# Performance work log

Measured on AMD Instinct MI355X. Metric: run time of the kernel, lower is better.

The kernel has to match this reference:

```python
import jax, jax.numpy as jnp
import numpy as np

B, S, C, H = 256, 512, 64, 128  # batch, seq_len, input channels, LSTM hidden


def setup_inputs() -> dict:
    key = jax.random.key(0)
    ks = jax.random.split(key, 9)
    s = 1.0 / np.sqrt(H)  # torch nn.LSTM init: U(-1/sqrt(H), 1/sqrt(H))
    u = lambda k, shape: jax.random.uniform(k, shape, jnp.float32, -s, s)
    return {
        "x": jax.random.normal(ks[0], (B, S, C), jnp.float32),
        # layer 0 (input size C)
        "Wih0": u(ks[1], (4 * H, C)),
        "Whh0": u(ks[2], (4 * H, H)),
        "bih0": u(ks[3], (4 * H,)),
        "bhh0": u(ks[4], (4 * H,)),
        # layer 1 (input size H)
        "Wih1": u(ks[5], (4 * H, H)),
        "Whh1": u(ks[6], (4 * H, H)),
        "bih1": u(ks[7], (4 * H,)),
        "bhh1": u(ks[8], (4 * H,)),
    }


def _lstm_layer(x, Wih, Whh, bih, bhh):
    """x: (S, B, in) -> outputs h_t for all t: (S, B, H). Torch gate order i,f,g,o."""
    Hh = Whh.shape[1]
    # Input-to-hidden GEMM hoisted out of the recurrence (batched over S).
    xg = jnp.einsum('sbc,gc->sbg', x, Wih) + bih + bhh  # (S, B, 4H)

    def step(carry, xt):
        h, c = carry
        g = xt + h @ Whh.T  # (B, 4H)
        i, f, gg, o = jnp.split(g, 4, axis=-1)
        i = jax.nn.sigmoid(i)
        f = jax.nn.sigmoid(f)
        gg = jnp.tanh(gg)
        o = jax.nn.sigmoid(o)
        c = f * c + i * gg
        h = o * jnp.tanh(c)
        return (h, c), h

    h0 = jnp.zeros((x.shape[1], Hh), x.dtype)
    _, ys = jax.lax.scan(step, (h0, h0), xg)
    return ys


def reference(x, Wih0, Whh0, bih0, bhh0, Wih1, Whh1, bih1, bhh1):
    xs = jnp.transpose(x, (1, 0, 2))  # (B,S,C) -> (S,B,C), matching x.permute(1,0,2)
    y1 = _lstm_layer(xs, Wih0, Whh0, bih0, bhh0)
    y2 = _lstm_layer(y1, Wih1, Whh1, bih1, bhh1)
    return y2[-1]  # x[-1, :, :]: last timestep of top layer, (B, H)
```

## Files before the change

kernel.cpp:

```cpp
#include <hip/hip_runtime.h>
#include <cstdint>
#include <cstddef>


#define S_LEN 512
#define B_SZ  256
#define C_IN  64
#define HDIM  128
#define NBLK  64
#define XG_TSTRIDE (64 * 512 * 4)

using short4v = __attribute__((ext_vector_type(4))) short;
using short8  = __attribute__((ext_vector_type(8))) short;
using float4v = __attribute__((ext_vector_type(4))) float;

template<bool V> struct Flag { static constexpr bool value = V; };

__device__ __forceinline__ unsigned short f2b(float f) {
    union { float f; unsigned int u; } v; v.f = f;
    unsigned int u = v.u;
    return (unsigned short)((u + 0x7FFFu + ((u >> 16) & 1u)) >> 16);
}
__device__ __forceinline__ float b2f(unsigned short s) {
    union { unsigned int u; float f; } v; v.u = ((unsigned int)s) << 16;
    return v.f;
}
__device__ __forceinline__ float sig_(float x) {
    return __builtin_amdgcn_rcpf(1.0f + __builtin_amdgcn_exp2f(x * -1.442695041f));
}
__device__ __forceinline__ float tanh_(float x) {
    return 1.0f - 2.0f * __builtin_amdgcn_rcpf(1.0f + __builtin_amdgcn_exp2f(x * 2.885390082f));
}
__device__ __forceinline__ short8 load8_f2b(const float* s) {
    const float4v f0 = *(const float4v*)s;
    const float4v f1 = *(const float4v*)(s + 4);
    short8 t;
#pragma unroll
    for (int e = 0; e < 4; ++e) {
        t[e]     = (short)f2b(f0[e]);
        t[e + 4] = (short)f2b(f1[e]);
    }
    return t;
}

__global__ void conv_kernel(const float* __restrict__ whh0,
                            const float* __restrict__ wih1, const float* __restrict__ whh1,
                            const float* __restrict__ bih1, const float* __restrict__ bhh1,
                            unsigned short* __restrict__ whh0_b, unsigned short* __restrict__ wih1_b,
                            unsigned short* __restrict__ whh1_b, float* __restrict__ bias1) {
    int i = blockIdx.x * blockDim.x + threadIdx.x;
    if (i < 4 * HDIM * HDIM) {
        whh0_b[i] = f2b(whh0[i]);
        wih1_b[i] = f2b(wih1[i]);
        whh1_b[i] = f2b(whh1[i]);
    }
    if (i < 4 * HDIM) bias1[i] = bih1[i] + bhh1[i];
}

__global__ __launch_bounds__(512, 2)
void xg_gemm(const float* __restrict__ x, const float* __restrict__ wih0,
             const float* __restrict__ bih0, const float* __restrict__ bhh0,
             unsigned short* __restrict__ xg) {
    const int tid = threadIdx.x;
    const int w = tid >> 6, L = tid & 63, q = L >> 4, r = L & 15;
    const int blk = blockIdx.x, tch = blockIdx.y;
    const int boff = blk * 4, j = w * 16 + r;
    const int rowload = r >> 2;

    short8 wf[4][2]; float bias_s[4];
#pragma unroll
    for (int g = 0; g < 4; ++g) {
        const int nrow = g * HDIM + j;
#pragma unroll
        for (int kk = 0; kk < 2; ++kk)
            wf[g][kk] = load8_f2b(wih0 + (size_t)nrow * C_IN + kk * 32 + q * 8);
        bias_s[g] = bih0[nrow] + bhh0[nrow];
    }

    const float* px = x + ((size_t)(boff + rowload) * S_LEN + (size_t)tch * 32) * C_IN + q * 8;
    unsigned short* po = xg + ((size_t)(tch * 32) * NBLK + blk) * 2048 + (size_t)tid * 4;

    for (int tt = 0; tt < 32; ++tt) {
        short8 xa[2];
#pragma unroll
        for (int kk = 0; kk < 2; ++kk) xa[kk] = load8_f2b(px + kk * 32);
        float4v a[4];
#pragma unroll
        for (int g = 0; g < 4; ++g) a[g] = (float4v){bias_s[g], 0.f, 0.f, 0.f};
#pragma unroll
        for (int kk = 0; kk < 2; ++kk)
#pragma unroll
            for (int g = 0; g < 4; ++g)
                a[g] = __builtin_amdgcn_mfma_f32_16x16x32_bf16(xa[kk], wf[g][kk], a[g], 0, 0, 0);
        short4v o;
#pragma unroll
        for (int g = 0; g < 4; ++g) o[g] = (short)f2b(a[g][0]);
        *(short4v*)po = o;
        px += C_IN;
        po += XG_TSTRIDE;
    }
}

__global__ __launch_bounds__(512, 2)
void lstm_fused(const unsigned short* __restrict__ whh0_b,
                const unsigned short* __restrict__ wih1_b,
                const unsigned short* __restrict__ whh1_b,
                const float* __restrict__ bias1,
                const unsigned short* __restrict__ xg,
                float* __restrict__ out) {
    __shared__ __align__(16) unsigned short hbuf[4 * 2048];
    const int tid = threadIdx.x;
    const int w = tid >> 6, L = tid & 63, q = L >> 4, r = L & 15;
    const int blk = blockIdx.x;
    const int boff = blk * 4, j = w * 16 + r;

    short8 whh0[4][4], wih1[4][4], whh1[4][4];
    float b1s[4];
#pragma unroll
    for (int g = 0; g < 4; ++g) {
        const size_t nrow = (size_t)(g * HDIM + j);
#pragma unroll
        for (int kk = 0; kk < 4; ++kk) {
            whh0[g][kk] = *(const short8*)(whh0_b + nrow * HDIM + kk * 32 + q * 8);
            wih1[g][kk] = *(const short8*)(wih1_b + nrow * HDIM + kk * 32 + q * 8);
            whh1[g][kk] = *(const short8*)(whh1_b + nrow * HDIM + kk * 32 + q * 8);
        }
        b1s[g] = bias1[g * HDIM + j];
    }
#pragma unroll
    for (int g = 0; g < 4; ++g) {
        asm volatile("" : "+v"(whh0[g][0]), "+v"(whh0[g][1]), "+v"(whh0[g][2]), "+v"(whh0[g][3]));
        asm volatile("" : "+v"(wih1[g][0]), "+v"(wih1[g][1]), "+v"(wih1[g][2]), "+v"(wih1[g][3]));
        asm volatile("" : "+v"(whh1[g][0]), "+v"(whh1[g][1]), "+v"(whh1[g][2]), "+v"(whh1[g][3]));
    }

    for (int idx = tid; idx < 4 * 1024; idx += 512) ((unsigned int*)hbuf)[idx] = 0u;

    float cf0 = 0.f, cf1 = 0.f;
    const int rred = r & ~3;
    const int rdoff = q * 128 + rred * 8;
    const int chunkbase = (j >> 3) * 128 + (j & 7);
    const int wslot = chunkbase + (4 * q) * 8;
    float* fout = out + (size_t)(boff + q) * HDIM + j;

    const unsigned short* pxg = xg + (size_t)blk * 2048 + (size_t)tid * 4;
    short4v xgA = *(const short4v*)pxg;
    pxg += XG_TSTRIDE;
    short4v xgB;

    __syncthreads();

    auto step = [&](auto D0_, auto D1_, auto FIN_,
                    unsigned short* r0, unsigned short* w0,
                    unsigned short* r1, unsigned short* w1,
                    short4v& xc, short4v& xn) {
        constexpr bool D0  = decltype(D0_)::value;
        constexpr bool D1  = decltype(D1_)::value;
        constexpr bool FIN = decltype(FIN_)::value;

        if constexpr (!FIN) {
            xn = *(const short4v*)pxg;
            pxg += XG_TSTRIDE;
        }

        if constexpr (D0) {
            float4v a0[4];
#pragma unroll
            for (int g = 0; g < 4; ++g)
                a0[g] = (float4v){b2f((unsigned short)xc[g]), 0.f, 0.f, 0.f};
            __builtin_amdgcn_s_setprio(1);
#pragma unroll
            for (int kk = 0; kk < 4; ++kk) {
                const short8 h0f = *(const short8*)(r0 + kk * 512 + rdoff);
#pragma unroll
                for (int g = 0; g < 4; ++g)
                    a0[g] = __builtin_amdgcn_mfma_f32_16x16x32_bf16(h0f, whh0[g][kk], a0[g], 0, 0, 0);
            }
            __builtin_amdgcn_s_setprio(0);
            {
                const float iv = sig_(a0[0][0]);
                const float fv = sig_(a0[1][0]);
                const float gv = tanh_(a0[2][0]);
                const float ov = sig_(a0[3][0]);
                cf0 = fv * cf0 + iv * gv;
                w0[wslot] = f2b(ov * tanh_(cf0));
            }
        }

        if constexpr (D1) {
            float4v a1[4];
#pragma unroll
            for (int g = 0; g < 4; ++g) a1[g] = (float4v){b1s[g], 0.f, 0.f, 0.f};
            __builtin_amdgcn_s_setprio(1);
#pragma unroll
            for (int kk = 0; kk < 4; ++kk) {
                const short8 hif = *(const short8*)(r0 + kk * 512 + rdoff);
#pragma unroll
                for (int g = 0; g < 4; ++g)
                    a1[g] = __builtin_amdgcn_mfma_f32_16x16x32_bf16(hif, wih1[g][kk], a1[g], 0, 0, 0);
            }
#pragma unroll
            for (int kk = 0; kk < 4; ++kk) {
                const short8 h1f = *(const short8*)(r1 + kk * 512 + rdoff);
#pragma unroll
                for (int g = 0; g < 4; ++g)
                    a1[g] = __builtin_amdgcn_mfma_f32_16x16x32_bf16(h1f, whh1[g][kk], a1[g], 0, 0, 0);
            }
            __builtin_amdgcn_s_setprio(0);
            {
                const float iv = sig_(a1[0][0]);
                const float fv = sig_(a1[1][0]);
                const float gv = tanh_(a1[2][0]);
                const float ov = sig_(a1[3][0]);
                cf1 = fv * cf1 + iv * gv;
                const float hv = ov * tanh_(cf1);
                if constexpr (FIN) fout[0] = hv;
                else w1[wslot] = f2b(hv);
            }
        }

        if constexpr (!FIN)
            asm volatile("s_waitcnt lgkmcnt(0)\n\ts_barrier" ::: "memory");
    };

    unsigned short* h0A = hbuf;
    unsigned short* h0B = hbuf + 2048;
    unsigned short* h1A = hbuf + 4096;
    unsigned short* h1B = hbuf + 6144;
    using T = Flag<true>; using F = Flag<false>;

    step(T{}, F{}, F{}, h0A, h0B, h1A, h1B, xgA, xgB);
#pragma unroll 1
    for (int k = 0; k < 255; ++k) {
        step(T{}, T{}, F{}, h0B, h0A, h1B, h1A, xgB, xgA);
        step(T{}, T{}, F{}, h0A, h0B, h1A, h1B, xgA, xgB);
    }
    step(T{}, T{}, F{}, h0B, h0A, h1B, h1A, xgB, xgA);
    step(F{}, T{}, T{}, h0A, h0B, h1A, h1B, xgA, xgB);
}


extern "C" void kernel_launch(void* const* d_in, const int* in_sizes, int n_in,
                              void* d_out, int out_size, void* d_ws, size_t ws_size,
                              hipStream_t stream) {
    const float* x    = (const float*)d_in[0];
    const float* wih0 = (const float*)d_in[1];
    const float* whh0 = (const float*)d_in[2];
    const float* bih0 = (const float*)d_in[3];
    const float* bhh0 = (const float*)d_in[4];
    const float* wih1 = (const float*)d_in[5];
    const float* whh1 = (const float*)d_in[6];
    const float* bih1 = (const float*)d_in[7];
    const float* bhh1 = (const float*)d_in[8];

    char* ws = (char*)d_ws;
    unsigned short* whh0_b = (unsigned short*)(ws + 0);
    unsigned short* wih1_b = (unsigned short*)(ws + 131072);
    unsigned short* whh1_b = (unsigned short*)(ws + 262144);
    float*          bias1  = (float*)(ws + 393216);
    unsigned short* xgp    = (unsigned short*)(ws + 524288);

    conv_kernel<<<256, 256, 0, stream>>>(whh0, wih1, whh1, bih1, bhh1,
                                         whh0_b, wih1_b, whh1_b, bias1);
    xg_gemm<<<dim3(NBLK, 16), 512, 0, stream>>>(x, wih0, bih0, bhh0, xgp);
    lstm_fused<<<NBLK, 512, 0, stream>>>(whh0_b, wih1_b, whh1_b, bias1, xgp,
                                         (float*)d_out);
}
```

Before: 694.5 us.

## Pre-convert input to bf16, prefetch in xg GEMM, pin LSTM weights in AGPRs

The conv kernel now also converts the whole input x to bf16 in a grid-stride loop, using a larger grid. The input-projection GEMM then reads bf16 directly, software-prefetches the next timestep's operands, and runs twice as many blocks over half as many timesteps each. In the fused LSTM kernel the register-pinning asm constraints move the weight fragments from VGPRs to AGPRs to ease VGPR pressure. The tradeoff is an extra full pass over x plus a 16 MB bf16 staging buffer in workspace, and possible copies if the MFMA operands must move out of AGPRs.

```diff
diff --git a/kernel.cpp b/kernel.cpp
--- a/kernel.cpp
+++ b/kernel.cpp
@@ -43,22 +43,33 @@
     return t;
 }
 
-__global__ void conv_kernel(const float* __restrict__ whh0,
+__global__ void conv_kernel(const float* __restrict__ x,
+                            const float* __restrict__ whh0,
                             const float* __restrict__ wih1, const float* __restrict__ whh1,
                             const float* __restrict__ bih1, const float* __restrict__ bhh1,
                             unsigned short* __restrict__ whh0_b, unsigned short* __restrict__ wih1_b,
-                            unsigned short* __restrict__ whh1_b, float* __restrict__ bias1) {
-    int i = blockIdx.x * blockDim.x + threadIdx.x;
+                            unsigned short* __restrict__ whh1_b, float* __restrict__ bias1,
+                            unsigned short* __restrict__ xb) {
+    const int i = blockIdx.x * blockDim.x + threadIdx.x;
     if (i < 4 * HDIM * HDIM) {
         whh0_b[i] = f2b(whh0[i]);
         wih1_b[i] = f2b(wih1[i]);
         whh1_b[i] = f2b(whh1[i]);
     }
     if (i < 4 * HDIM) bias1[i] = bih1[i] + bhh1[i];
+    const int nvec = (B_SZ * S_LEN * C_IN) / 4;
+    const int stride = gridDim.x * blockDim.x;
+    for (int idx = i; idx < nvec; idx += stride) {
+        const float4v f = ((const float4v*)x)[idx];
+        short4v o;
+#pragma unroll
+        for (int e = 0; e < 4; ++e) o[e] = (short)f2b(f[e]);
+        ((short4v*)xb)[idx] = o;
+    }
 }
 
 __global__ __launch_bounds__(512, 2)
-void xg_gemm(const float* __restrict__ x, const float* __restrict__ wih0,
+void xg_gemm(const unsigned short* __restrict__ xb, const float* __restrict__ wih0,
              const float* __restrict__ bih0, const float* __restrict__ bhh0,
              unsigned short* __restrict__ xg) {
     const int tid = threadIdx.x;
@@ -77,13 +88,22 @@
         bias_s[g] = bih0[nrow] + bhh0[nrow];
     }
 
-    const float* px = x + ((size_t)(boff + rowload) * S_LEN + (size_t)tch * 32) * C_IN + q * 8;
-    unsigned short* po = xg + ((size_t)(tch * 32) * NBLK + blk) * 2048 + (size_t)tid * 4;
-
-    for (int tt = 0; tt < 32; ++tt) {
-        short8 xa[2];
-#pragma unroll
-        for (int kk = 0; kk < 2; ++kk) xa[kk] = load8_f2b(px + kk * 32);
+    const unsigned short* px = xb + ((size_t)(boff + rowload) * S_LEN + (size_t)tch * 16) * C_IN + q * 8;
+    unsigned short* po = xg + ((size_t)(tch * 16) * NBLK + blk) * 2048 + (size_t)tid * 4;
+
+    short8 cur[2];
+#pragma unroll
+    for (int kk = 0; kk < 2; ++kk) cur[kk] = *(const short8*)(px + kk * 32);
+    px += C_IN;
+
+#pragma unroll
+    for (int tt = 0; tt < 16; ++tt) {
+        short8 nxt[2];
+        if (tt < 15) {
+#pragma unroll
+            for (int kk = 0; kk < 2; ++kk) nxt[kk] = *(const short8*)(px + kk * 32);
+        }
+        px += C_IN;
         float4v a[4];
 #pragma unroll
         for (int g = 0; g < 4; ++g) a[g] = (float4v){bias_s[g], 0.f, 0.f, 0.f};
@@ -91,13 +111,13 @@
         for (int kk = 0; kk < 2; ++kk)
 #pragma unroll
             for (int g = 0; g < 4; ++g)
-                a[g] = __builtin_amdgcn_mfma_f32_16x16x32_bf16(xa[kk], wf[g][kk], a[g], 0, 0, 0);
+                a[g] = __builtin_amdgcn_mfma_f32_16x16x32_bf16(cur[kk], wf[g][kk], a[g], 0, 0, 0);
         short4v o;
 #pragma unroll
         for (int g = 0; g < 4; ++g) o[g] = (short)f2b(a[g][0]);
         *(short4v*)po = o;
-        px += C_IN;
         po += XG_TSTRIDE;
+        cur[0] = nxt[0]; cur[1] = nxt[1];
     }
 }
 
@@ -129,9 +149,9 @@
     }
 #pragma unroll
     for (int g = 0; g < 4; ++g) {
-        asm volatile("" : "+v"(whh0[g][0]), "+v"(whh0[g][1]), "+v"(whh0[g][2]), "+v"(whh0[g][3]));
-        asm volatile("" : "+v"(wih1[g][0]), "+v"(wih1[g][1]), "+v"(wih1[g][2]), "+v"(wih1[g][3]));
-        asm volatile("" : "+v"(whh1[g][0]), "+v"(whh1[g][1]), "+v"(whh1[g][2]), "+v"(whh1[g][3]));
+        asm volatile("" : "+a"(whh0[g][0]), "+a"(whh0[g][1]), "+a"(whh0[g][2]), "+a"(whh0[g][3]));
+        asm volatile("" : "+a"(wih1[g][0]), "+a"(wih1[g][1]), "+a"(wih1[g][2]), "+a"(wih1[g][3]));
+        asm volatile("" : "+a"(whh1[g][0]), "+a"(whh1[g][1]), "+a"(whh1[g][2]), "+a"(whh1[g][3]));
     }
 
     for (int idx = tid; idx < 4 * 1024; idx += 512) ((unsigned int*)hbuf)[idx] = 0u;
@@ -258,11 +278,12 @@
     unsigned short* wih1_b = (unsigned short*)(ws + 131072);
     unsigned short* whh1_b = (unsigned short*)(ws + 262144);
     float*          bias1  = (float*)(ws + 393216);
-    unsigned short* xgp    = (unsigned short*)(ws + 524288);
-
-    conv_kernel<<<256, 256, 0, stream>>>(whh0, wih1, whh1, bih1, bhh1,
-                                         whh0_b, wih1_b, whh1_b, bias1);
-    xg_gemm<<<dim3(NBLK, 16), 512, 0, stream>>>(x, wih0, bih0, bhh0, xgp);
+    unsigned short* xb     = (unsigned short*)(ws + 458752);
+    unsigned short* xgp    = (unsigned short*)(ws + 17235968);
+
+    conv_kernel<<<4096, 256, 0, stream>>>(x, whh0, wih1, whh1, bih1, bhh1,
+                                          whh0_b, wih1_b, whh1_b, bias1, xb);
+    xg_gemm<<<dim3(NBLK, 32), 512, 0, stream>>>(xb, wih0, bih0, bhh0, xgp);
     lstm_fused<<<NBLK, 512, 0, stream>>>(whh0_b, wih1_b, whh1_b, bias1, xgp,
                                          (float*)d_out);
 }
```

Result: no change. 697.4 us (+0.4%).
